# Optimization experiments

Measured on AMD Instinct MI355X. Metric: run time of the kernel, lower is better.

## Reference

```python
import jax, jax.numpy as jnp
import numpy as np

NUM_GROUPS = 9
POWER_P = 4.0
B = 8192

def setup_inputs() -> dict:
    key = jax.random.key(0)
    k1, k2, k3 = jax.random.split(key, 3)
    return {
        "logits_tox": jax.random.normal(k1, (B, 1), dtype=jnp.float32),
        "y_tox": jax.random.uniform(k2, (B, 1), dtype=jnp.float32),
        "y_id": jax.random.uniform(k3, (B, NUM_GROUPS), dtype=jnp.float32),
    }

def reference(logits_tox, y_tox, y_id):
    logits = logits_tox[:, 0]                      # [B]
    is_toxic = y_tox[:, 0] >= 0.5                  # [B] bool
    # D[i, j] = softplus(-(logits[i] - logits[j])) = softplus(logits[j] - logits[i])
    # row index i plays the 'pos' role, column index j plays the 'neg' role.
    D = jax.nn.softplus(logits[None, :] - logits[:, None])  # [B, B]

    in_group = (y_id >= 0.5).T                     # [G, B]
    tox = is_toxic[None, :]                        # [1, B]
    dt = logits.dtype
    sub_pos = (in_group & tox).astype(dt)          # [G, B]
    sub_neg = (in_group & ~tox).astype(dt)
    bg_pos = (~in_group & tox).astype(dt)
    bg_neg = (~in_group & ~tox).astype(dt)

    # three pair types: (sub_pos, sub_neg), (bg_pos, sub_neg), (sub_pos, bg_neg)
    pos_masks = jnp.stack([sub_pos, bg_pos, sub_pos])   # [3, G, B]
    neg_masks = jnp.stack([sub_neg, sub_neg, bg_neg])   # [3, G, B]

    num = jnp.einsum('tgi,ij,tgj->tg', pos_masks, D, neg_masks)  # [3, G]
    cnt = pos_masks.sum(-1) * neg_masks.sum(-1)                  # [3, G] n_pos*n_neg
    valid = cnt > 0                                              # pair type contributes only if both sides nonempty
    type_loss = num / jnp.maximum(cnt, 1.0)

    n_valid = valid.astype(dt).sum(0)                            # [G]
    group_loss = (type_loss * valid.astype(dt)).sum(0) / jnp.maximum(n_valid, 1.0)
    gv = (n_valid > 0).astype(dt)                                # [G] group validity
    n_groups = jnp.maximum(gv.sum(), 1.0)

    # power-mean aggregation (power_p = 4 > 1)
    mean_p = (jnp.power(group_loss, POWER_P) * gv).sum() / n_groups
    loss = jnp.power(mean_p, 1.0 / POWER_P)
    return jnp.where(gv.sum() > 0, loss, jnp.array(0.0, dt))
```

## Files before the change

kernel.cpp:

```cpp
#include <hip/hip_runtime.h>
#include <math.h>

#define NG 9
#define NBLK 1024
#define CHROWS 256
#define NCHMAX 256
#define JT 32
#define ITILE 512
#define LOG2E 1.4426950408889634f
#define LN2   0.6931471805599453f

__global__ __launch_bounds__(256) void k_classify(
    const float* __restrict__ logits, const float* __restrict__ ytox,
    const float* __restrict__ yid, int B,
    int* __restrict__ cntT, int* __restrict__ cntN,
    int* __restrict__ gTc, int* __restrict__ gNc,
    float2* __restrict__ iTmp, float2* __restrict__ jTmp) {

    __shared__ int wT[4], wN[4], oT[4], oN[4];
    __shared__ int gT[4][NG], gN[4][NG];

    const int tid = threadIdx.x, lane = tid & 63, wave = tid >> 6;
    const int c = blockIdx.x;
    const int row = c * CHROWS + tid;
    const bool v = row < B;

    float l = 0.f; bool tox = false, non = false; int m = 0;
    if (v) {
        l = logits[row] * LOG2E;
        tox = ytox[row] >= 0.5f;
        non = !tox;
#pragma unroll
        for (int g = 0; g < NG; ++g)
            if (yid[row * NG + g] >= 0.5f) m |= 1 << g;
    }
    const unsigned long long bTox = __ballot(tox), bNon = __ballot(non);
    const unsigned long long lt = (1ull << lane) - 1ull;
    const int pT = __popcll(bTox & lt), pN = __popcll(bNon & lt);
    if (lane == 0) { wT[wave] = __popcll(bTox); wN[wave] = __popcll(bNon); }
#pragma unroll
    for (int g = 0; g < NG; ++g) {
        const unsigned long long bt = __ballot(tox && ((m >> g) & 1));
        const unsigned long long bn = __ballot(non && ((m >> g) & 1));
        if (lane == 0) { gT[wave][g] = __popcll(bt); gN[wave][g] = __popcll(bn); }
    }
    __syncthreads();
    if (tid == 0) {
        int a = 0, b = 0;
#pragma unroll
        for (int w = 0; w < 4; ++w) { oT[w] = a; a += wT[w]; oN[w] = b; b += wN[w]; }
        cntT[c] = a; cntN[c] = b;
    }
    __syncthreads();
    if (tox) iTmp[c * CHROWS + oT[wave] + pT] = make_float2(l, __int_as_float(m));
    if (non) jTmp[c * CHROWS + oN[wave] + pN] = make_float2(l, __int_as_float(m));
    if (tid < NG)
        gTc[c * NG + tid] = gT[0][tid] + gT[1][tid] + gT[2][tid] + gT[3][tid];
    else if (tid >= 64 && tid < 64 + NG) {
        const int g = tid - 64;
        gNc[c * NG + g] = gN[0][g] + gN[1][g] + gN[2][g] + gN[3][g];
    }
}

__global__ __launch_bounds__(256, 4) void k_pairs(
    const int* __restrict__ cntT, const int* __restrict__ cntN,
    const float2* __restrict__ iTmp, const float2* __restrict__ jTmp,
    int B, float* __restrict__ part) {

    __shared__ int offT[NCHMAX + 1], offN[NCHMAX + 1];
    __shared__ float2 jS[JT];
    __shared__ float red[4][27];
    __shared__ float acc[27];

    const int tid = threadIdx.x, lane = tid & 63, wave = tid >> 6;
    const int blk = blockIdx.x;
    const int nCh = (B + CHROWS - 1) / CHROWS;

    for (int c = tid; c < nCh; c += 256) { offT[c + 1] = cntT[c]; offN[c + 1] = cntN[c]; }
    if (tid == 0) { offT[0] = 0; offN[0] = 0; }
    __syncthreads();
    if (tid == 0)
        for (int c = 0; c < nCh; ++c) { offT[c + 1] += offT[c]; offN[c + 1] += offN[c]; }
    if (tid < 27) acc[tid] = 0.f;
    __syncthreads();
    const int nI = offT[nCh], nJ = offN[nCh];

    auto findChunk = [&](const int* off, int k) {
        int lo = 0, hi = nCh;
        while (hi - lo > 1) { const int mid = (lo + hi) >> 1; if (off[mid] <= k) lo = mid; else hi = mid; }
        return lo;
    };

    float li0 = 1e30f, li1 = 1e30f;
    int mi0 = 0, mi1 = 0;
    float Ra0 = 0.f, Ra1 = 0.f;
    float Rg0[NG], Rg1[NG];
#pragma unroll
    for (int g = 0; g < NG; ++g) { Rg0[g] = 0.f; Rg1[g] = 0.f; }

    auto flush = [&]() {
#pragma unroll
        for (int g = 0; g < NG; ++g) {
            const bool i0 = (mi0 >> g) & 1, i1 = (mi1 >> g) & 1;
            float x0 = (i0 ? Rg0[g] : 0.f) + (i1 ? Rg1[g] : 0.f);
            float x1 = (i0 ? 0.f : Rg0[g]) + (i1 ? 0.f : Rg1[g]);
            float x2 = (i0 ? (Ra0 - Rg0[g]) : 0.f) + (i1 ? (Ra1 - Rg1[g]) : 0.f);
#pragma unroll
            for (int off = 32; off > 0; off >>= 1) {
                x0 += __shfl_xor(x0, off, 64);
                x1 += __shfl_xor(x1, off, 64);
                x2 += __shfl_xor(x2, off, 64);
            }
            if (lane == 0) {
                red[wave][g] = x0; red[wave][NG + g] = x1; red[wave][2 * NG + g] = x2;
            }
        }
        __syncthreads();
        if (tid < 27)
            acc[tid] += red[0][tid] + red[1][tid] + red[2][tid] + red[3][tid];
    };

    const int nbI = (nI + ITILE - 1) / ITILE;
    const int nbJ = (nJ + JT - 1) / JT;
    const int nT = nbI * nbJ;

    int prev_bi = -1;
    for (int t = blk; t < nT; t += NBLK) {
        const int bi = t % nbI, bj = t / nbI;
        if (bi != prev_bi) {
            if (prev_bi >= 0) flush();
            const int k0 = bi * ITILE + tid, k1 = k0 + 256;
            float2 a0 = make_float2(1e30f, 0.f), a1 = make_float2(1e30f, 0.f);
            if (k0 < nI) { const int c = findChunk(offT, k0); a0 = iTmp[c * CHROWS + (k0 - offT[c])]; }
            if (k1 < nI) { const int c = findChunk(offT, k1); a1 = iTmp[c * CHROWS + (k1 - offT[c])]; }
            li0 = a0.x; mi0 = __float_as_int(a0.y);
            li1 = a1.x; mi1 = __float_as_int(a1.y);
            Ra0 = 0.f; Ra1 = 0.f;
#pragma unroll
            for (int g = 0; g < NG; ++g) { Rg0[g] = 0.f; Rg1[g] = 0.f; }
            prev_bi = bi;
        }
        const int jbeg = bj * JT;
        const int jcnt = min(JT, nJ - jbeg);
        __syncthreads();
        if (tid < jcnt) {
            const int k = jbeg + tid;
            const int c = findChunk(offN, k);
            jS[tid] = jTmp[c * CHROWS + (k - offN[c])];
        }
        __syncthreads();
#pragma unroll 4
        for (int k = 0; k < jcnt; ++k) {
            const float2 jv = jS[k];
            const float lj = jv.x;
            const int mj = __builtin_amdgcn_readfirstlane(__float_as_int(jv.y));
            const float s0 = __builtin_amdgcn_logf(1.f + __builtin_amdgcn_exp2f(lj - li0));
            const float s1 = __builtin_amdgcn_logf(1.f + __builtin_amdgcn_exp2f(lj - li1));
            Ra0 += s0; Ra1 += s1;
#pragma unroll
            for (int g = 0; g < NG; ++g) {
                const float bg = ((mj >> g) & 1) ? 1.f : 0.f;
                Rg0[g] = fmaf(bg, s0, Rg0[g]);
                Rg1[g] = fmaf(bg, s1, Rg1[g]);
            }
        }
    }
    if (prev_bi >= 0) flush();
    if (tid < 27) part[tid * NBLK + blk] = acc[tid];
}

__global__ __launch_bounds__(512) void k_final(
    const float* __restrict__ part, const int* __restrict__ cntT,
    const int* __restrict__ cntN, const int* __restrict__ gTc,
    const int* __restrict__ gNc, int B, float* __restrict__ out) {

    __shared__ float fin[27];
    __shared__ int cTs[NG], cNs[NG], nTs, nNs;
    const int tid = threadIdx.x, lane = tid & 63, wave = tid >> 6;
    const int nCh = (B + CHROWS - 1) / CHROWS;

    for (int r = wave; r < 27; r += 8) {
        float s = 0.f;
#pragma unroll
        for (int q = 0; q < NBLK / 64; ++q) s += part[r * NBLK + (q << 6) + lane];
#pragma unroll
        for (int off = 32; off > 0; off >>= 1) s += __shfl_xor(s, off, 64);
        if (lane == 0) fin[r] = s * LN2;
    }
    if (tid < NG) {
        int s = 0;
        for (int c = 0; c < nCh; ++c) s += gTc[c * NG + tid];
        cTs[tid] = s;
    } else if (tid >= 64 && tid < 64 + NG) {
        const int g = tid - 64;
        int s = 0;
        for (int c = 0; c < nCh; ++c) s += gNc[c * NG + g];
        cNs[g] = s;
    } else if (tid == 128) {
        int s = 0;
        for (int c = 0; c < nCh; ++c) s += cntT[c];
        nTs = s;
    } else if (tid == 192) {
        int s = 0;
        for (int c = 0; c < nCh; ++c) s += cntN[c];
        nNs = s;
    }
    __syncthreads();
    if (tid == 0) {
        const long long nT64 = nTs, nN64 = nNs;
        double accd = 0.0; int ngv = 0;
        for (int g = 0; g < NG; ++g) {
            const long long cT = cTs[g], cN = cNs[g];
            const long long c0 = cT * cN;
            const long long c1 = (nT64 - cT) * cN;
            const long long c2 = cT * (nN64 - cN);
            const double t0 = (double)fin[g]          / (double)(c0 > 0 ? c0 : 1);
            const double t1 = (double)fin[NG + g]     / (double)(c1 > 0 ? c1 : 1);
            const double t2 = (double)fin[2 * NG + g] / (double)(c2 > 0 ? c2 : 1);
            const int nv = (c0 > 0) + (c1 > 0) + (c2 > 0);
            const double gl = ((c0 > 0 ? t0 : 0.0) + (c1 > 0 ? t1 : 0.0) +
                               (c2 > 0 ? t2 : 0.0)) / (double)(nv > 0 ? nv : 1);
            if (nv > 0) { const double g2 = gl * gl; accd += g2 * g2; ++ngv; }
        }
        const double mp = accd / (double)(ngv > 0 ? ngv : 1);
        const double loss = sqrt(sqrt(mp));
        out[0] = (float)(ngv > 0 ? loss : 0.0);
    }
}

extern "C" void kernel_launch(void* const* d_in, const int* in_sizes, int n_in,
                              void* d_out, int out_size, void* d_ws, size_t ws_size,
                              hipStream_t stream) {
    const float* logits = (const float*)d_in[0];
    const float* ytox   = (const float*)d_in[1];
    const float* yid    = (const float*)d_in[2];
    const int B = in_sizes[0];
    const int nCh = (B + CHROWS - 1) / CHROWS;

    char* ws = (char*)d_ws;
    int* cntT = (int*)ws;
    int* cntN = cntT + NCHMAX;
    int* gTc  = cntN + NCHMAX;
    int* gNc  = gTc + NCHMAX * NG;
    float2* iTmp = (float2*)(gNc + NCHMAX * NG);
    float2* jTmp = iTmp + B;
    float*  part = (float*)(jTmp + B);

    k_classify<<<dim3(nCh), dim3(256), 0, stream>>>(logits, ytox, yid, B,
                                                    cntT, cntN, gTc, gNc, iTmp, jTmp);
    k_pairs<<<dim3(NBLK), dim3(256), 0, stream>>>(cntT, cntN, iTmp, jTmp, B, part);
    k_final<<<dim3(1), dim3(512), 0, stream>>>(part, cntT, cntN, gTc, gNc, B,
                                               (float*)d_out);
}
```

Baseline: 91.86 us.

## Fuse final reduction into pair kernel via last-block ticket and packed float2 math

Removes the separate final-reduction kernel launch. Each pair block now stores its partials atomically and takes a ticket, and the last block to finish performs the global reduction and computes the loss. The ticket counter is reset by the classify kernel. The pair kernel's inner loop is also rewritten with two-wide float vectors so the compiler can emit packed FP32 add/FMA for the two rows per thread, with the unroll factor lowered from 4 to 2. The cost is an extra atomic per block and a serialized tail in one block.

```diff
diff --git a/kernel.cpp b/kernel.cpp
--- a/kernel.cpp
+++ b/kernel.cpp
@@ -10,12 +10,15 @@
 #define LOG2E 1.4426950408889634f
 #define LN2   0.6931471805599453f
 
+typedef float f32x2 __attribute__((ext_vector_type(2)));
+
 __global__ __launch_bounds__(256) void k_classify(
     const float* __restrict__ logits, const float* __restrict__ ytox,
     const float* __restrict__ yid, int B,
     int* __restrict__ cntT, int* __restrict__ cntN,
     int* __restrict__ gTc, int* __restrict__ gNc,
-    float2* __restrict__ iTmp, float2* __restrict__ jTmp) {
+    float2* __restrict__ iTmp, float2* __restrict__ jTmp,
+    int* __restrict__ ticket) {
 
     __shared__ int wT[4], wN[4], oT[4], oN[4];
     __shared__ int gT[4][NG], gN[4][NG];
@@ -24,6 +27,8 @@
     const int c = blockIdx.x;
     const int row = c * CHROWS + tid;
     const bool v = row < B;
+
+    if (c == 0 && tid == 0) ticket[0] = 0;
 
     float l = 0.f; bool tox = false, non = false; int m = 0;
     if (v) {
@@ -64,8 +69,10 @@
 
 __global__ __launch_bounds__(256, 4) void k_pairs(
     const int* __restrict__ cntT, const int* __restrict__ cntN,
+    const int* __restrict__ gTc, const int* __restrict__ gNc,
     const float2* __restrict__ iTmp, const float2* __restrict__ jTmp,
-    int B, float* __restrict__ part) {
+    int B, float* __restrict__ part, int* __restrict__ ticket,
+    float* __restrict__ out) {
 
     __shared__ int offT[NCHMAX + 1], offN[NCHMAX + 1];
     __shared__ float2 jS[JT];
@@ -78,10 +85,10 @@
 
     for (int c = tid; c < nCh; c += 256) { offT[c + 1] = cntT[c]; offN[c + 1] = cntN[c]; }
     if (tid == 0) { offT[0] = 0; offN[0] = 0; }
+    if (tid < 27) acc[tid] = 0.f;
     __syncthreads();
     if (tid == 0)
         for (int c = 0; c < nCh; ++c) { offT[c + 1] += offT[c]; offN[c + 1] += offN[c]; }
-    if (tid < 27) acc[tid] = 0.f;
     __syncthreads();
     const int nI = offT[nCh], nJ = offN[nCh];
 
@@ -91,20 +98,21 @@
         return lo;
     };
 
-    float li0 = 1e30f, li1 = 1e30f;
+    f32x2 li = {1e30f, 1e30f};
     int mi0 = 0, mi1 = 0;
-    float Ra0 = 0.f, Ra1 = 0.f;
-    float Rg0[NG], Rg1[NG];
-#pragma unroll
-    for (int g = 0; g < NG; ++g) { Rg0[g] = 0.f; Rg1[g] = 0.f; }
+    f32x2 Ra = {0.f, 0.f};
+    f32x2 Rg[NG];
+#pragma unroll
+    for (int g = 0; g < NG; ++g) Rg[g] = (f32x2){0.f, 0.f};
 
     auto flush = [&]() {
 #pragma unroll
         for (int g = 0; g < NG; ++g) {
             const bool i0 = (mi0 >> g) & 1, i1 = (mi1 >> g) & 1;
-            float x0 = (i0 ? Rg0[g] : 0.f) + (i1 ? Rg1[g] : 0.f);
-            float x1 = (i0 ? 0.f : Rg0[g]) + (i1 ? 0.f : Rg1[g]);
-            float x2 = (i0 ? (Ra0 - Rg0[g]) : 0.f) + (i1 ? (Ra1 - Rg1[g]) : 0.f);
+            const float r0 = Rg[g].x, r1 = Rg[g].y;
+            float x0 = (i0 ? r0 : 0.f) + (i1 ? r1 : 0.f);
+            float x1 = (i0 ? 0.f : r0) + (i1 ? 0.f : r1);
+            float x2 = (i0 ? (Ra.x - r0) : 0.f) + (i1 ? (Ra.y - r1) : 0.f);
 #pragma unroll
             for (int off = 32; off > 0; off >>= 1) {
                 x0 += __shfl_xor(x0, off, 64);
@@ -133,11 +141,11 @@
             float2 a0 = make_float2(1e30f, 0.f), a1 = make_float2(1e30f, 0.f);
             if (k0 < nI) { const int c = findChunk(offT, k0); a0 = iTmp[c * CHROWS + (k0 - offT[c])]; }
             if (k1 < nI) { const int c = findChunk(offT, k1); a1 = iTmp[c * CHROWS + (k1 - offT[c])]; }
-            li0 = a0.x; mi0 = __float_as_int(a0.y);
-            li1 = a1.x; mi1 = __float_as_int(a1.y);
-            Ra0 = 0.f; Ra1 = 0.f;
-#pragma unroll
-            for (int g = 0; g < NG; ++g) { Rg0[g] = 0.f; Rg1[g] = 0.f; }
+            li.x = a0.x; mi0 = __float_as_int(a0.y);
+            li.y = a1.x; mi1 = __float_as_int(a1.y);
+            Ra = (f32x2){0.f, 0.f};
+#pragma unroll
+            for (int g = 0; g < NG; ++g) Rg[g] = (f32x2){0.f, 0.f};
             prev_bi = bi;
         }
         const int jbeg = bj * JT;
@@ -149,40 +157,51 @@
             jS[tid] = jTmp[c * CHROWS + (k - offN[c])];
         }
         __syncthreads();
-#pragma unroll 4
+#pragma unroll 2
         for (int k = 0; k < jcnt; ++k) {
             const float2 jv = jS[k];
-            const float lj = jv.x;
             const int mj = __builtin_amdgcn_readfirstlane(__float_as_int(jv.y));
-            const float s0 = __builtin_amdgcn_logf(1.f + __builtin_amdgcn_exp2f(lj - li0));
-            const float s1 = __builtin_amdgcn_logf(1.f + __builtin_amdgcn_exp2f(lj - li1));
-            Ra0 += s0; Ra1 += s1;
+            const f32x2 ljv = {jv.x, jv.x};
+            const f32x2 d = ljv - li;
+            f32x2 e;
+            e.x = __builtin_amdgcn_exp2f(d.x);
+            e.y = __builtin_amdgcn_exp2f(d.y);
+            const f32x2 one = {1.f, 1.f};
+            const f32x2 tpe = e + one;
+            f32x2 s;
+            s.x = __builtin_amdgcn_logf(tpe.x);
+            s.y = __builtin_amdgcn_logf(tpe.y);
+            Ra = Ra + s;
 #pragma unroll
             for (int g = 0; g < NG; ++g) {
                 const float bg = ((mj >> g) & 1) ? 1.f : 0.f;
-                Rg0[g] = fmaf(bg, s0, Rg0[g]);
-                Rg1[g] = fmaf(bg, s1, Rg1[g]);
+                const f32x2 bgv = {bg, bg};
+                Rg[g] = __builtin_elementwise_fma(bgv, s, Rg[g]);
             }
         }
     }
     if (prev_bi >= 0) flush();
-    if (tid < 27) part[tid * NBLK + blk] = acc[tid];
-}
-
-__global__ __launch_bounds__(512) void k_final(
-    const float* __restrict__ part, const int* __restrict__ cntT,
-    const int* __restrict__ cntN, const int* __restrict__ gTc,
-    const int* __restrict__ gNc, int B, float* __restrict__ out) {
+
+    if (tid < 27)
+        __hip_atomic_store(&part[tid * NBLK + blk], acc[tid],
+                           __ATOMIC_RELAXED, __HIP_MEMORY_SCOPE_AGENT);
+    __shared__ int isLast;
+    if (tid == 0) {
+        const int old = __hip_atomic_fetch_add(ticket, 1, __ATOMIC_ACQ_REL,
+                                               __HIP_MEMORY_SCOPE_AGENT);
+        isLast = (old == NBLK - 1);
+    }
+    __syncthreads();
+    if (!isLast) return;
 
     __shared__ float fin[27];
     __shared__ int cTs[NG], cNs[NG], nTs, nNs;
-    const int tid = threadIdx.x, lane = tid & 63, wave = tid >> 6;
-    const int nCh = (B + CHROWS - 1) / CHROWS;
-
-    for (int r = wave; r < 27; r += 8) {
+    for (int r = wave; r < 27; r += 4) {
         float s = 0.f;
 #pragma unroll
-        for (int q = 0; q < NBLK / 64; ++q) s += part[r * NBLK + (q << 6) + lane];
+        for (int q = 0; q < NBLK / 64; ++q)
+            s += __hip_atomic_load(&part[r * NBLK + (q << 6) + lane],
+                                   __ATOMIC_RELAXED, __HIP_MEMORY_SCOPE_AGENT);
 #pragma unroll
         for (int off = 32; off > 0; off >>= 1) s += __shfl_xor(s, off, 64);
         if (lane == 0) fin[r] = s * LN2;
@@ -197,13 +216,9 @@
         for (int c = 0; c < nCh; ++c) s += gNc[c * NG + g];
         cNs[g] = s;
     } else if (tid == 128) {
-        int s = 0;
-        for (int c = 0; c < nCh; ++c) s += cntT[c];
-        nTs = s;
+        nTs = nI;
     } else if (tid == 192) {
-        int s = 0;
-        for (int c = 0; c < nCh; ++c) s += cntN[c];
-        nNs = s;
+        nNs = nJ;
     }
     __syncthreads();
     if (tid == 0) {
@@ -242,13 +257,13 @@
     int* cntN = cntT + NCHMAX;
     int* gTc  = cntN + NCHMAX;
     int* gNc  = gTc + NCHMAX * NG;
-    float2* iTmp = (float2*)(gNc + NCHMAX * NG);
+    int* ticket = gNc + NCHMAX * NG;
+    float2* iTmp = (float2*)(ticket + 32);
     float2* jTmp = iTmp + B;
     float*  part = (float*)(jTmp + B);
 
-    k_classify<<<dim3(nCh), dim3(256), 0, stream>>>(logits, ytox, yid, B,
-                                                    cntT, cntN, gTc, gNc, iTmp, jTmp);
-    k_pairs<<<dim3(NBLK), dim3(256), 0, stream>>>(cntT, cntN, iTmp, jTmp, B, part);
-    k_final<<<dim3(1), dim3(512), 0, stream>>>(part, cntT, cntN, gTc, gNc, B,
-                                               (float*)d_out);
+    k_classify<<<dim3(nCh), dim3(256), 0, stream>>>(
+        logits, ytox, yid, B, cntT, cntN, gTc, gNc, iTmp, jTmp, ticket);
+    k_pairs<<<dim3(NBLK), dim3(256), 0, stream>>>(
+        cntT, cntN, gTc, gNc, iTmp, jTmp, B, part, ticket, (float*)d_out);
 }
```

New measurement: 95.43 us. 1.04x slower.
